# Kernel tuning notes

Hardware: AMD Instinct MI355X
Metric: run time of the kernel (lower is better)

Reference implementation:

```python
import jax, jax.numpy as jnp
import numpy as np

B, T, D = 1, 2048, 4096
H, HKV, HD = 32, 8, 128   # attention heads, KV heads, head_dim
R, RANK = 64, 16          # virtual KV tokens, LoRA rank
EPS = 1e-6


def setup_inputs() -> dict:
    key = jax.random.key(0)
    ks = jax.random.split(key, 12)
    inp = {
        "hidden_states": jax.random.normal(ks[0], (B, T, D), jnp.float32),
        "virtual_keys": jax.random.normal(ks[1], (B, HKV, R, HD), jnp.float32),
        "virtual_values": jax.random.normal(ks[2], (B, HKV, R, HD), jnp.float32),
        "Wq": jax.random.normal(ks[3], (D, H * HD), jnp.float32) * 0.02,
        "Wk": jax.random.normal(ks[4], (D, HKV * HD), jnp.float32) * 0.02,
        "Wv": jax.random.normal(ks[5], (D, HKV * HD), jnp.float32) * 0.02,
        "Wo": jax.random.normal(ks[6], (H * HD, D), jnp.float32) * 0.02,
        "q_norm_w": jnp.ones((HD,), jnp.float32),
        "k_norm_w": jnp.ones((HD,), jnp.float32),
        "lora_k_A": jax.random.normal(ks[7], (HD, RANK), jnp.float32) / np.sqrt(HD),
        "lora_k_B": jax.random.normal(ks[8], (RANK, HD), jnp.float32) * 0.02,
        "lora_v_A": jax.random.normal(ks[9], (HD, RANK), jnp.float32) / np.sqrt(HD),
        "lora_v_B": jax.random.normal(ks[10], (RANK, HD), jnp.float32) * 0.02,
        "scale_k": jnp.float32(0.1),
        "scale_v": jnp.float32(0.1),
    }
    # additive causal mask (B,1,T,T)
    neg = jnp.finfo(jnp.float32).min
    idx = jnp.arange(T)
    mask = jnp.where(idx[None, :] <= idx[:, None], 0.0, neg).astype(jnp.float32)
    inp["attention_mask"] = jnp.broadcast_to(mask[None, None], (B, 1, T, T))
    # rotary embeddings (T, HD)
    inv_freq = 1.0 / (10000.0 ** (jnp.arange(0, HD, 2, dtype=jnp.float32) / HD))
    freqs = jnp.outer(jnp.arange(T, dtype=jnp.float32), inv_freq)
    emb = jnp.concatenate([freqs, freqs], axis=-1)
    inp["cos"], inp["sin"] = jnp.cos(emb), jnp.sin(emb)
    return inp


def _rms_norm(x, w):
    xf = x.astype(jnp.float32)
    y = xf * jax.lax.rsqrt(jnp.mean(xf * xf, axis=-1, keepdims=True) + EPS)
    return y.astype(x.dtype) * w


def _rotate_half(x):
    x1, x2 = jnp.split(x, 2, axis=-1)
    return jnp.concatenate([-x2, x1], axis=-1)


def reference(hidden_states, virtual_keys, virtual_values, Wq, Wk, Wv, Wo,
              q_norm_w, k_norm_w, lora_k_A, lora_k_B, lora_v_A, lora_v_B,
              scale_k, scale_v, attention_mask, cos, sin):
    b, t, d = hidden_states.shape
    head_dim = q_norm_w.shape[0]
    scaling = head_dim ** -0.5

    # ---- KVLoRAAdapter: K' = K + s_k * (K @ A_k @ B_k), same for V ----
    vk = virtual_keys + scale_k * ((virtual_keys @ lora_k_A) @ lora_k_B)
    vv = virtual_values + scale_v * ((virtual_values @ lora_v_A) @ lora_v_B)

    # ---- Qwen3 attention projections with per-head RMSNorm ----
    q = _rms_norm((hidden_states @ Wq).reshape(b, t, -1, head_dim), q_norm_w).transpose(0, 2, 1, 3)  # (B,H,T,hd)
    k = _rms_norm((hidden_states @ Wk).reshape(b, t, -1, head_dim), k_norm_w).transpose(0, 2, 1, 3)  # (B,HKV,T,hd)
    v = (hidden_states @ Wv).reshape(b, t, -1, head_dim).transpose(0, 2, 1, 3)                       # (B,HKV,T,hd)

    # ---- RoPE ----
    c, s = cos[None, None], sin[None, None]
    q = q * c + _rotate_half(q) * s
    k = k * c + _rotate_half(k) * s

    # ---- prepend adapted virtual KV ----
    r = vk.shape[2]
    k = jnp.concatenate([vk.astype(k.dtype), k], axis=2)  # (B,HKV,r+T,hd)
    v = jnp.concatenate([vv.astype(v.dtype), v], axis=2)
    virtual_mask = jnp.zeros((b, 1, t, r), attention_mask.dtype)
    full_mask = jnp.concatenate([virtual_mask, attention_mask], axis=-1)  # (B,1,T,r+T)

    # ---- repeat_kv (GQA) ----
    groups = q.shape[1] // k.shape[1]
    k = jnp.repeat(k, groups, axis=1)
    v = jnp.repeat(v, groups, axis=1)

    # ---- attention ----
    attn = jnp.einsum('bhqd,bhkd->bhqk', q, k) * scaling + full_mask
    attn = jax.nn.softmax(attn.astype(jnp.float32), axis=-1).astype(q.dtype)
    out = jnp.einsum('bhqk,bhkd->bhqd', attn, v)
    out = out.transpose(0, 2, 1, 3).reshape(b, t, -1)
    return out @ Wo
```

## Files before the change

kernel.cpp:

```cpp
#include <hip/hip_runtime.h>

typedef unsigned short u16;
typedef __attribute__((ext_vector_type(8))) unsigned short u16x8;
typedef __attribute__((ext_vector_type(8))) short s16x8;
typedef __attribute__((ext_vector_type(4))) float f32x4;

__device__ __forceinline__ float bf2f(u16 v) {
    return __uint_as_float(((unsigned int)v) << 16);
}
__device__ __forceinline__ u16 f2bf(float f) {
    unsigned int u = __float_as_uint(f);
    return (u16)((u + 0x7FFFu + ((u >> 16) & 1u)) >> 16);
}

__global__ __launch_bounds__(256) void cvt_bf16_kernel(const float* __restrict__ src,
                                                       u16* __restrict__ dst, int n8) {
    int i = blockIdx.x * 256 + threadIdx.x;
    if (i >= n8) return;
    const float4* s4 = (const float4*)src;
    float4 a = s4[i * 2];
    float4 b = s4[i * 2 + 1];
    u16x8 o;
    o[0] = f2bf(a.x); o[1] = f2bf(a.y); o[2] = f2bf(a.z); o[3] = f2bf(a.w);
    o[4] = f2bf(b.x); o[5] = f2bf(b.y); o[6] = f2bf(b.z); o[7] = f2bf(b.w);
    *(u16x8*)(dst + (size_t)i * 8) = o;
}

__global__ __launch_bounds__(256) void tcvt_kernel(const float* __restrict__ src,
                                                   u16* __restrict__ dst, int K, int N) {
    __shared__ float T[32][33];
    int k0 = blockIdx.x * 32, n0 = blockIdx.y * 32;
    int r = threadIdx.x >> 5, c = threadIdx.x & 31;
#pragma unroll
    for (int it = 0; it < 4; ++it)
        T[it * 8 + r][c] = src[(size_t)(k0 + it * 8 + r) * N + n0 + c];
    __syncthreads();
#pragma unroll
    for (int it = 0; it < 4; ++it)
        dst[(size_t)(n0 + it * 8 + r) * K + k0 + c] = f2bf(T[c][it * 8 + r]);
}

__global__ __launch_bounds__(128) void lora_kv_kernel(
    const float* __restrict__ vk, const float* __restrict__ vv,
    const float* __restrict__ kA, const float* __restrict__ kB,
    const float* __restrict__ vA, const float* __restrict__ vB,
    const float* __restrict__ skp, const float* __restrict__ svp,
    u16* __restrict__ k_full, u16* __restrict__ v_t) {
    __shared__ float row[128];
    __shared__ float tv[16];
    int h = blockIdx.x >> 6, r = blockIdx.x & 63;
    int d = threadIdx.x;

    row[d] = vk[(size_t)(h * 64 + r) * 128 + d];
    __syncthreads();
    if (d < 16) {
        float acc = 0.f;
        for (int i = 0; i < 128; ++i) acc += row[i] * kA[i * 16 + d];
        tv[d] = acc;
    }
    __syncthreads();
    float acc = 0.f;
#pragma unroll
    for (int j = 0; j < 16; ++j) acc += tv[j] * kB[j * 128 + d];
    float outk = row[d] + skp[0] * acc;
    k_full[((size_t)h * 2112 + r) * 128 + d] = f2bf(outk);
    __syncthreads();

    row[d] = vv[(size_t)(h * 64 + r) * 128 + d];
    __syncthreads();
    if (d < 16) {
        float a2 = 0.f;
        for (int i = 0; i < 128; ++i) a2 += row[i] * vA[i * 16 + d];
        tv[d] = a2;
    }
    __syncthreads();
    float a3 = 0.f;
#pragma unroll
    for (int j = 0; j < 16; ++j) a3 += tv[j] * vB[j * 128 + d];
    float outv = row[d] + svp[0] * a3;
    v_t[((size_t)h * 128 + d) * 2112 + r] = f2bf(outv);
}

template <int OF32>
__global__ __launch_bounds__(256) void gemm_bt_kernel(const u16* __restrict__ A,
                                                      const u16* __restrict__ B,
                                                      void* __restrict__ Cv,
                                                      int M, int N, int K, int ldc) {
    __shared__ u16 As[128][40];
    __shared__ u16 Bs[128][40];
    int tid = threadIdx.x;
    int w = tid >> 6, l = tid & 63, lr = l & 15, lg = l >> 4;
    int m0 = blockIdx.x * 128, n0 = blockIdx.y * 128;
    int wr = (w >> 1) * 64, wc = (w & 1) * 64;
    int trow = tid >> 2, tcol = (tid & 3) * 8;

    const u16* Ag = A + (size_t)(m0 + trow) * K + tcol;
    const u16* Bg = B + (size_t)(n0 + trow) * K + tcol;

    u16x8 ra0 = *(const u16x8*)Ag;
    u16x8 ra1 = *(const u16x8*)(Ag + (size_t)64 * K);
    u16x8 rb0 = *(const u16x8*)Bg;
    u16x8 rb1 = *(const u16x8*)(Bg + (size_t)64 * K);

    f32x4 acc[4][4] = {};
    int NT = K >> 5;
    for (int kt = 0; kt < NT; ++kt) {
        __syncthreads();
        *(u16x8*)&As[trow][tcol] = ra0;
        *(u16x8*)&As[trow + 64][tcol] = ra1;
        *(u16x8*)&Bs[trow][tcol] = rb0;
        *(u16x8*)&Bs[trow + 64][tcol] = rb1;
        if (kt + 1 < NT) {
            int kb = (kt + 1) * 32;
            ra0 = *(const u16x8*)(Ag + kb);
            ra1 = *(const u16x8*)(Ag + kb + (size_t)64 * K);
            rb0 = *(const u16x8*)(Bg + kb);
            rb1 = *(const u16x8*)(Bg + kb + (size_t)64 * K);
        }
        __syncthreads();
        s16x8 af[4], bfr[4];
#pragma unroll
        for (int m = 0; m < 4; ++m) af[m] = *(const s16x8*)&As[wr + m * 16 + lr][lg * 8];
#pragma unroll
        for (int n = 0; n < 4; ++n) bfr[n] = *(const s16x8*)&Bs[wc + n * 16 + lr][lg * 8];
#pragma unroll
        for (int m = 0; m < 4; ++m)
#pragma unroll
            for (int n = 0; n < 4; ++n)
                acc[m][n] = __builtin_amdgcn_mfma_f32_16x16x32_bf16(af[m], bfr[n], acc[m][n], 0, 0, 0);
    }

#pragma unroll
    for (int m = 0; m < 4; ++m)
#pragma unroll
        for (int n = 0; n < 4; ++n)
#pragma unroll
            for (int j = 0; j < 4; ++j) {
                int row = m0 + wr + m * 16 + lg * 4 + j;
                int col = n0 + wc + n * 16 + lr;
                float v = acc[m][n][j];
                if (OF32)
                    ((float*)Cv)[(size_t)row * ldc + col] = v;
                else
                    ((u16*)Cv)[(size_t)row * ldc + col] = f2bf(v);
            }
}

__global__ __launch_bounds__(256) void qnorm_rope_kernel(const u16* __restrict__ qkv,
                                                         const float* __restrict__ qw,
                                                         const float* __restrict__ cosb,
                                                         const float* __restrict__ sinb,
                                                         u16* __restrict__ qf) {
    int w = threadIdx.x >> 6, l = threadIdx.x & 63;
    int idx = blockIdx.x * 4 + w;
    int t = idx >> 5, h = idx & 31;
    const u16* src = qkv + (size_t)t * 6144 + h * 128;
    float x1 = bf2f(src[l]), x2 = bf2f(src[l + 64]);
    float ss = x1 * x1 + x2 * x2;
#pragma unroll
    for (int d = 1; d < 64; d <<= 1) ss += __shfl_xor(ss, d, 64);
    float rinv = rsqrtf(ss * (1.0f / 128.0f) + 1e-6f);
    float y1 = x1 * rinv * qw[l], y2 = x2 * rinv * qw[l + 64];
    float c1 = cosb[t * 128 + l], s1 = sinb[t * 128 + l];
    float c2 = cosb[t * 128 + l + 64], s2 = sinb[t * 128 + l + 64];
    const float sc = 0.08838834764831845f;
    u16* dst = qf + (size_t)t * 4096 + h * 128;
    dst[l] = f2bf((y1 * c1 - y2 * s1) * sc);
    dst[l + 64] = f2bf((y2 * c2 + y1 * s2) * sc);
}

__global__ __launch_bounds__(256) void kvnorm_rope_kernel(const u16* __restrict__ qkv,
                                                          const float* __restrict__ kw,
                                                          const float* __restrict__ cosb,
                                                          const float* __restrict__ sinb,
                                                          u16* __restrict__ k_full,
                                                          u16* __restrict__ v_t) {
    __shared__ u16 VT[32][136];
    int h = blockIdx.x >> 6;
    int t0 = (blockIdx.x & 63) * 32;
    int tid = threadIdx.x;
    int w = tid >> 6, l = tid & 63;

    for (int it = 0; it < 8; ++it) {
        int t = t0 + w * 8 + it;
        const u16* src = qkv + (size_t)t * 6144 + 4096 + h * 128;
        float x1 = bf2f(src[l]), x2 = bf2f(src[l + 64]);
        float ss = x1 * x1 + x2 * x2;
#pragma unroll
        for (int d = 1; d < 64; d <<= 1) ss += __shfl_xor(ss, d, 64);
        float rinv = rsqrtf(ss * (1.0f / 128.0f) + 1e-6f);
        float y1 = x1 * rinv * kw[l], y2 = x2 * rinv * kw[l + 64];
        float c1 = cosb[t * 128 + l], s1 = sinb[t * 128 + l];
        float c2 = cosb[t * 128 + l + 64], s2 = sinb[t * 128 + l + 64];
        u16* dst = k_full + ((size_t)h * 2112 + 64 + t) * 128;
        dst[l] = f2bf(y1 * c1 - y2 * s1);
        dst[l + 64] = f2bf(y2 * c2 + y1 * s2);
    }

    {
        int tr = tid >> 3, c0 = (tid & 7) * 16;
        const u16* src = qkv + (size_t)(t0 + tr) * 6144 + 5120 + h * 128 + c0;
        *(u16x8*)&VT[tr][c0] = *(const u16x8*)src;
        *(u16x8*)&VT[tr][c0 + 8] = *(const u16x8*)(src + 8);
    }
    __syncthreads();
    {
        int d = tid >> 1, th = (tid & 1) * 16;
        u16x8 a, b;
#pragma unroll
        for (int i = 0; i < 8; ++i) { a[i] = VT[th + i][d]; b[i] = VT[th + 8 + i][d]; }
        u16* dst = v_t + ((size_t)h * 128 + d) * 2112 + 64 + t0 + th;
        *(u16x8*)dst = a;
        *(u16x8*)(dst + 8) = b;
    }
}

__global__ __launch_bounds__(256) void attn_kernel(const u16* __restrict__ qf,
                                                   const u16* __restrict__ k_full,
                                                   const u16* __restrict__ v_t,
                                                   u16* __restrict__ attn_out) {
    __shared__ u16 Ks[64][136];
    __shared__ u16 Vs[128][72];
    __shared__ u16 Pw[4][16][72];

    int h = blockIdx.x >> 5;
    int qt = 31 - (blockIdx.x & 31);
    int q0 = qt * 64;
    int kvh = h >> 2;
    int tid = threadIdx.x, w = tid >> 6, l = tid & 63;
    int lr = l & 15, lg = l >> 4;

    s16x8 qfr[4];
    const u16* qbase = qf + (size_t)(q0 + w * 16 + lr) * 4096 + h * 128 + lg * 8;
#pragma unroll
    for (int ks = 0; ks < 4; ++ks) qfr[ks] = *(const s16x8*)(qbase + ks * 32);

    f32x4 o[8] = {};
    float mrun[4], lrun[4];
#pragma unroll
    for (int j = 0; j < 4; ++j) { mrun[j] = -1e30f; lrun[j] = 0.f; }

    int nt = q0 / 64 + 2;
    const u16* Kg = k_full + (size_t)kvh * 2112 * 128;
    const u16* Vg = v_t + (size_t)kvh * 128 * 2112;

    for (int tile = 0; tile < nt; ++tile) {
        int kv0 = tile * 64;
        __syncthreads();
#pragma unroll
        for (int c = 0; c < 4; ++c) {
            int kk = tid + c * 256;
            int row = kk >> 4, col = (kk & 15) * 8;
            *(u16x8*)&Ks[row][col] = *(const u16x8*)(Kg + (size_t)(kv0 + row) * 128 + col);
        }
#pragma unroll
        for (int c = 0; c < 4; ++c) {
            int kk = tid + c * 256;
            int row = kk >> 3, col = (kk & 7) * 8;
            *(u16x8*)&Vs[row][col] = *(const u16x8*)(Vg + (size_t)row * 2112 + kv0 + col);
        }
        __syncthreads();

        f32x4 s[4] = {};
#pragma unroll
        for (int ks = 0; ks < 4; ++ks) {
#pragma unroll
            for (int n = 0; n < 4; ++n) {
                s16x8 b = *(const s16x8*)&Ks[n * 16 + lr][ks * 32 + lg * 8];
                s[n] = __builtin_amdgcn_mfma_f32_16x16x32_bf16(qfr[ks], b, s[n], 0, 0, 0);
            }
        }

        if (tile == nt - 1) {
#pragma unroll
            for (int n = 0; n < 4; ++n) {
                int kvi = kv0 + n * 16 + lr;
                if (kvi >= 64) {
                    int kreal = kvi - 64;
#pragma unroll
                    for (int j = 0; j < 4; ++j) {
                        int qi = q0 + w * 16 + lg * 4 + j;
                        if (kreal > qi) s[n][j] = -1e30f;
                    }
                }
            }
        }

#pragma unroll
        for (int j = 0; j < 4; ++j) {
            float mx = fmaxf(fmaxf(s[0][j], s[1][j]), fmaxf(s[2][j], s[3][j]));
            mx = fmaxf(mx, __shfl_xor(mx, 1, 64));
            mx = fmaxf(mx, __shfl_xor(mx, 2, 64));
            mx = fmaxf(mx, __shfl_xor(mx, 4, 64));
            mx = fmaxf(mx, __shfl_xor(mx, 8, 64));
            float mnew = fmaxf(mrun[j], mx);
            float scl = __expf(mrun[j] - mnew);
            mrun[j] = mnew;
            lrun[j] *= scl;
#pragma unroll
            for (int nf = 0; nf < 8; ++nf) o[nf][j] *= scl;
            float psum = 0.f;
#pragma unroll
            for (int n = 0; n < 4; ++n) {
                float p = __expf(s[n][j] - mnew);
                s[n][j] = p;
                psum += p;
            }
            lrun[j] += psum;
        }

#pragma unroll
        for (int n = 0; n < 4; ++n)
#pragma unroll
            for (int j = 0; j < 4; ++j)
                Pw[w][lg * 4 + j][n * 16 + lr] = f2bf(s[n][j]);

#pragma unroll
        for (int ks2 = 0; ks2 < 2; ++ks2) {
            s16x8 pa = *(const s16x8*)&Pw[w][lr][ks2 * 32 + lg * 8];
#pragma unroll
            for (int nf = 0; nf < 8; ++nf) {
                s16x8 vb = *(const s16x8*)&Vs[nf * 16 + lr][ks2 * 32 + lg * 8];
                o[nf] = __builtin_amdgcn_mfma_f32_16x16x32_bf16(pa, vb, o[nf], 0, 0, 0);
            }
        }
    }

    float rinv[4];
#pragma unroll
    for (int j = 0; j < 4; ++j) {
        float ls = lrun[j];
        ls += __shfl_xor(ls, 1, 64);
        ls += __shfl_xor(ls, 2, 64);
        ls += __shfl_xor(ls, 4, 64);
        ls += __shfl_xor(ls, 8, 64);
        rinv[j] = 1.0f / ls;
    }
#pragma unroll
    for (int nf = 0; nf < 8; ++nf)
#pragma unroll
        for (int j = 0; j < 4; ++j) {
            int row = q0 + w * 16 + lg * 4 + j;
            int col = h * 128 + nf * 16 + lr;
            attn_out[(size_t)row * 4096 + col] = f2bf(o[nf][j] * rinv[j]);
        }
}

extern "C" void kernel_launch(void* const* d_in, const int* in_sizes, int n_in,
                              void* d_out, int out_size, void* d_ws, size_t ws_size,
                              hipStream_t stream) {
    const float* hidden = (const float*)d_in[0];
    const float* vkeys = (const float*)d_in[1];
    const float* vvals = (const float*)d_in[2];
    const float* Wq = (const float*)d_in[3];
    const float* Wk = (const float*)d_in[4];
    const float* Wv = (const float*)d_in[5];
    const float* Wo = (const float*)d_in[6];
    const float* qnw = (const float*)d_in[7];
    const float* knw = (const float*)d_in[8];
    const float* lkA = (const float*)d_in[9];
    const float* lkB = (const float*)d_in[10];
    const float* lvA = (const float*)d_in[11];
    const float* lvB = (const float*)d_in[12];
    const float* skp = (const float*)d_in[13];
    const float* svp = (const float*)d_in[14];
    const float* cosb = (const float*)d_in[16];
    const float* sinb = (const float*)d_in[17];

    char* ws = (char*)d_ws;
    u16* hid_bf = (u16*)(ws);
    u16* WqT    = (u16*)(ws + 16777216);
    u16* WkT    = (u16*)(ws + 50331648);
    u16* WvT    = (u16*)(ws + 58720256);
    u16* WoT    = (u16*)(ws + 67108864);
    u16* qkv    = (u16*)(ws + 100663296);
    u16* qfin   = (u16*)(ws + 125829120);
    u16* kfull  = (u16*)(ws + 142606336);
    u16* vt     = (u16*)(ws + 146931712);
    u16* attn_o = hid_bf;

    cvt_bf16_kernel<<<4096, 256, 0, stream>>>(hidden, hid_bf, 1048576);
    tcvt_kernel<<<dim3(128, 128), 256, 0, stream>>>(Wq, WqT, 4096, 4096);
    tcvt_kernel<<<dim3(128, 32), 256, 0, stream>>>(Wk, WkT, 4096, 1024);
    tcvt_kernel<<<dim3(128, 32), 256, 0, stream>>>(Wv, WvT, 4096, 1024);
    tcvt_kernel<<<dim3(128, 128), 256, 0, stream>>>(Wo, WoT, 4096, 4096);

    lora_kv_kernel<<<512, 128, 0, stream>>>(vkeys, vvals, lkA, lkB, lvA, lvB, skp, svp,
                                            kfull, vt);

    gemm_bt_kernel<0><<<dim3(16, 48), 256, 0, stream>>>(hid_bf, WqT, qkv, 2048, 6144, 4096, 6144);

    qnorm_rope_kernel<<<16384, 256, 0, stream>>>(qkv, qnw, cosb, sinb, qfin);
    kvnorm_rope_kernel<<<512, 256, 0, stream>>>(qkv, knw, cosb, sinb, kfull, vt);

    attn_kernel<<<1024, 256, 0, stream>>>(qfin, kfull, vt, attn_o);

    gemm_bt_kernel<1><<<dim3(16, 32), 256, 0, stream>>>(attn_o, WoT, d_out, 2048, 4096, 4096, 4096);
}
```

Baseline: 657.6 us.

## Use direct-to-LDS double-buffered GEMM loads and rebalance flash attention

The GEMM now copies global memory straight into a double-buffered LDS tile with global_load_lds, replacing the register-staged single buffer, so the next tile loads while the current one computes. The attention kernel pairs a long and a short causal query tile per block to even out work, and swaps padded LDS rows for XOR-swizzled layouts to avoid bank conflicts. It also folds log2(e) into the Q scale so it can use exp2f, and skips the running-max rescale when the max has grown by no more than a set threshold. This risks LDS bank conflicts in the unpadded GEMM tiles, leaves half as many attention blocks, and relies on the lazy-rescale threshold staying numerically safe.

```diff
diff --git a/kernel.cpp b/kernel.cpp
--- a/kernel.cpp
+++ b/kernel.cpp
@@ -5,12 +5,18 @@
 typedef __attribute__((ext_vector_type(8))) short s16x8;
 typedef __attribute__((ext_vector_type(4))) float f32x4;
 
+typedef __attribute__((address_space(1))) void gvoid;
+typedef __attribute__((address_space(3))) void lvoid;
+
 __device__ __forceinline__ float bf2f(u16 v) {
     return __uint_as_float(((unsigned int)v) << 16);
 }
 __device__ __forceinline__ u16 f2bf(float f) {
     unsigned int u = __float_as_uint(f);
     return (u16)((u + 0x7FFFu + ((u >> 16) & 1u)) >> 16);
+}
+__device__ __forceinline__ void gload16(const void* g, void* l) {
+    __builtin_amdgcn_global_load_lds((gvoid*)g, (lvoid*)l, 16, 0, 0);
 }
 
 __global__ __launch_bounds__(256) void cvt_bf16_kernel(const float* __restrict__ src,
@@ -86,49 +92,55 @@
                                                       const u16* __restrict__ B,
                                                       void* __restrict__ Cv,
                                                       int M, int N, int K, int ldc) {
-    __shared__ u16 As[128][40];
-    __shared__ u16 Bs[128][40];
+    __shared__ u16 As[2][128][32];
+    __shared__ u16 Bs[2][128][32];
     int tid = threadIdx.x;
     int w = tid >> 6, l = tid & 63, lr = l & 15, lg = l >> 4;
     int m0 = blockIdx.x * 128, n0 = blockIdx.y * 128;
     int wr = (w >> 1) * 64, wc = (w & 1) * 64;
-    int trow = tid >> 2, tcol = (tid & 3) * 8;
-
-    const u16* Ag = A + (size_t)(m0 + trow) * K + tcol;
-    const u16* Bg = B + (size_t)(n0 + trow) * K + tcol;
-
-    u16x8 ra0 = *(const u16x8*)Ag;
-    u16x8 ra1 = *(const u16x8*)(Ag + (size_t)64 * K);
-    u16x8 rb0 = *(const u16x8*)Bg;
-    u16x8 rb1 = *(const u16x8*)(Bg + (size_t)64 * K);
+    int srow = tid >> 2, scol = (tid & 3) * 8;
+
+    const u16* Ag = A + (size_t)(m0 + srow) * K + scol;
+    const u16* Bg = B + (size_t)(n0 + srow) * K + scol;
+    size_t rstep = (size_t)64 * K;
 
     f32x4 acc[4][4] = {};
     int NT = K >> 5;
-    for (int kt = 0; kt < NT; ++kt) {
+
+#define STAGE_G(buf, kt)                                       \
+    do {                                                       \
+        int koff = (kt) * 32;                                  \
+        gload16(Ag + koff, &As[buf][srow][scol]);              \
+        gload16(Ag + koff + rstep, &As[buf][srow + 64][scol]); \
+        gload16(Bg + koff, &Bs[buf][srow][scol]);              \
+        gload16(Bg + koff + rstep, &Bs[buf][srow + 64][scol]); \
+    } while (0)
+
+#define COMPUTE_G(buf)                                                                     \
+    do {                                                                                   \
+        s16x8 af[4], bfr[4];                                                               \
+        _Pragma("unroll") for (int m = 0; m < 4; ++m)                                      \
+            af[m] = *(const s16x8*)&As[buf][wr + m * 16 + lr][lg * 8];                     \
+        _Pragma("unroll") for (int n = 0; n < 4; ++n)                                      \
+            bfr[n] = *(const s16x8*)&Bs[buf][wc + n * 16 + lr][lg * 8];                    \
+        _Pragma("unroll") for (int m = 0; m < 4; ++m)                                      \
+            _Pragma("unroll") for (int n = 0; n < 4; ++n)                                  \
+                acc[m][n] = __builtin_amdgcn_mfma_f32_16x16x32_bf16(af[m], bfr[n],         \
+                                                                    acc[m][n], 0, 0, 0);  \
+    } while (0)
+
+    STAGE_G(0, 0);
+    __syncthreads();
+    for (int kt = 0; kt < NT; kt += 2) {
+        if (kt + 1 < NT) STAGE_G(1, kt + 1);
+        COMPUTE_G(0);
         __syncthreads();
-        *(u16x8*)&As[trow][tcol] = ra0;
-        *(u16x8*)&As[trow + 64][tcol] = ra1;
-        *(u16x8*)&Bs[trow][tcol] = rb0;
-        *(u16x8*)&Bs[trow + 64][tcol] = rb1;
-        if (kt + 1 < NT) {
-            int kb = (kt + 1) * 32;
-            ra0 = *(const u16x8*)(Ag + kb);
-            ra1 = *(const u16x8*)(Ag + kb + (size_t)64 * K);
-            rb0 = *(const u16x8*)(Bg + kb);
-            rb1 = *(const u16x8*)(Bg + kb + (size_t)64 * K);
-        }
+        if (kt + 2 < NT) STAGE_G(0, kt + 2);
+        COMPUTE_G(1);
         __syncthreads();
-        s16x8 af[4], bfr[4];
-#pragma unroll
-        for (int m = 0; m < 4; ++m) af[m] = *(const s16x8*)&As[wr + m * 16 + lr][lg * 8];
-#pragma unroll
-        for (int n = 0; n < 4; ++n) bfr[n] = *(const s16x8*)&Bs[wc + n * 16 + lr][lg * 8];
-#pragma unroll
-        for (int m = 0; m < 4; ++m)
-#pragma unroll
-            for (int n = 0; n < 4; ++n)
-                acc[m][n] = __builtin_amdgcn_mfma_f32_16x16x32_bf16(af[m], bfr[n], acc[m][n], 0, 0, 0);
-    }
+    }
+#undef STAGE_G
+#undef COMPUTE_G
 
 #pragma unroll
     for (int m = 0; m < 4; ++m)
@@ -163,7 +175,7 @@
     float y1 = x1 * rinv * qw[l], y2 = x2 * rinv * qw[l + 64];
     float c1 = cosb[t * 128 + l], s1 = sinb[t * 128 + l];
     float c2 = cosb[t * 128 + l + 64], s2 = sinb[t * 128 + l + 64];
-    const float sc = 0.08838834764831845f;
+    const float sc = 0.08838834764831845f * 1.4426950408889634f;
     u16* dst = qf + (size_t)t * 4096 + h * 128;
     dst[l] = f2bf((y1 * c1 - y2 * s1) * sc);
     dst[l + 64] = f2bf((y2 * c2 + y1 * s2) * sc);
@@ -219,131 +231,152 @@
                                                    const u16* __restrict__ k_full,
                                                    const u16* __restrict__ v_t,
                                                    u16* __restrict__ attn_out) {
-    __shared__ u16 Ks[64][136];
-    __shared__ u16 Vs[128][72];
-    __shared__ u16 Pw[4][16][72];
-
-    int h = blockIdx.x >> 5;
-    int qt = 31 - (blockIdx.x & 31);
-    int q0 = qt * 64;
+    __shared__ u16 Ks[64][128];
+    __shared__ u16 Vs[128][64];
+    __shared__ u16 Pw[4][16][64];
+
+    int h = blockIdx.x >> 4;
+    int pr = blockIdx.x & 15;
     int kvh = h >> 2;
     int tid = threadIdx.x, w = tid >> 6, l = tid & 63;
     int lr = l & 15, lg = l >> 4;
-
-    s16x8 qfr[4];
-    const u16* qbase = qf + (size_t)(q0 + w * 16 + lr) * 4096 + h * 128 + lg * 8;
-#pragma unroll
-    for (int ks = 0; ks < 4; ++ks) qfr[ks] = *(const s16x8*)(qbase + ks * 32);
-
-    f32x4 o[8] = {};
-    float mrun[4], lrun[4];
-#pragma unroll
-    for (int j = 0; j < 4; ++j) { mrun[j] = -1e30f; lrun[j] = 0.f; }
-
-    int nt = q0 / 64 + 2;
     const u16* Kg = k_full + (size_t)kvh * 2112 * 128;
     const u16* Vg = v_t + (size_t)kvh * 128 * 2112;
 
-    for (int tile = 0; tile < nt; ++tile) {
-        int kv0 = tile * 64;
-        __syncthreads();
-#pragma unroll
-        for (int c = 0; c < 4; ++c) {
-            int kk = tid + c * 256;
-            int row = kk >> 4, col = (kk & 15) * 8;
-            *(u16x8*)&Ks[row][col] = *(const u16x8*)(Kg + (size_t)(kv0 + row) * 128 + col);
+    for (int seg = 0; seg < 2; ++seg) {
+        int qt = seg ? pr : 31 - pr;
+        int q0 = qt * 64;
+
+        s16x8 qfr[4];
+        const u16* qbase = qf + (size_t)(q0 + w * 16 + lr) * 4096 + h * 128 + lg * 8;
+#pragma unroll
+        for (int ks = 0; ks < 4; ++ks) qfr[ks] = *(const s16x8*)(qbase + ks * 32);
+
+        f32x4 o[8] = {};
+        float mrun[4], lrun[4];
+#pragma unroll
+        for (int j = 0; j < 4; ++j) { mrun[j] = -1e30f; lrun[j] = 0.f; }
+
+        int nt = qt + 2;
+        for (int tile = 0; tile < nt; ++tile) {
+            int kv0 = tile * 64;
+            __syncthreads();
+#pragma unroll
+            for (int c = 0; c < 4; ++c) {
+                int kk = tid + c * 256;
+                int row = kk >> 4, col = (kk & 15) * 8;
+                *(u16x8*)&Ks[row][col ^ ((row & 7) << 3)] =
+                    *(const u16x8*)(Kg + (size_t)(kv0 + row) * 128 + col);
+            }
+#pragma unroll
+            for (int c = 0; c < 4; ++c) {
+                int kk = tid + c * 256;
+                int row = kk >> 3, col = (kk & 7) * 8;
+                *(u16x8*)&Vs[row][col ^ ((row & 7) << 3)] =
+                    *(const u16x8*)(Vg + (size_t)row * 2112 + kv0 + col);
+            }
+            __syncthreads();
+
+            f32x4 s[4] = {};
+#pragma unroll
+            for (int ks = 0; ks < 4; ++ks) {
+#pragma unroll
+                for (int n = 0; n < 4; ++n) {
+                    s16x8 b = *(const s16x8*)&Ks[n * 16 + lr][(ks * 32 + lg * 8) ^ ((lr & 7) << 3)];
+                    s[n] = __builtin_amdgcn_mfma_f32_16x16x32_bf16(qfr[ks], b, s[n], 0, 0, 0);
+                }
+            }
+
+            if (tile == nt - 1) {
+#pragma unroll
+                for (int n = 0; n < 4; ++n) {
+                    int kvi = kv0 + n * 16 + lr;
+                    if (kvi >= 64) {
+                        int kreal = kvi - 64;
+#pragma unroll
+                        for (int j = 0; j < 4; ++j) {
+                            int qi = q0 + w * 16 + lg * 4 + j;
+                            if (kreal > qi) s[n][j] = -1e30f;
+                        }
+                    }
+                }
+            }
+
+            float tmx[4];
+            float growth = -3.0e38f;
+#pragma unroll
+            for (int j = 0; j < 4; ++j) {
+                float mx = fmaxf(fmaxf(s[0][j], s[1][j]), fmaxf(s[2][j], s[3][j]));
+                mx = fmaxf(mx, __shfl_xor(mx, 1, 64));
+                mx = fmaxf(mx, __shfl_xor(mx, 2, 64));
+                mx = fmaxf(mx, __shfl_xor(mx, 4, 64));
+                mx = fmaxf(mx, __shfl_xor(mx, 8, 64));
+                tmx[j] = mx;
+                growth = fmaxf(growth, mx - mrun[j]);
+            }
+            if (!__all(growth <= 11.5f)) {
+#pragma unroll
+                for (int j = 0; j < 4; ++j) {
+                    float mnew = fmaxf(mrun[j], tmx[j]);
+                    float scl = exp2f(mrun[j] - mnew);
+                    mrun[j] = mnew;
+                    lrun[j] *= scl;
+#pragma unroll
+                    for (int nf = 0; nf < 8; ++nf) o[nf][j] *= scl;
+                }
+            }
+#pragma unroll
+            for (int j = 0; j < 4; ++j) {
+                float psum = 0.f;
+#pragma unroll
+                for (int n = 0; n < 4; ++n) {
+                    float p = exp2f(s[n][j] - mrun[j]);
+                    s[n][j] = p;
+                    psum += p;
+                }
+                lrun[j] += psum;
+            }
+
+#pragma unroll
+            for (int n = 0; n < 4; ++n)
+#pragma unroll
+                for (int j = 0; j < 4; ++j) {
+                    int prow = lg * 4 + j;
+                    int pcol = n * 16 + lr;
+                    int pswz = (pcol & 7) | ((((pcol >> 3) ^ prow) & 7) << 3);
+                    Pw[w][prow][pswz] = f2bf(s[n][j]);
+                }
+
+#pragma unroll
+            for (int ks2 = 0; ks2 < 2; ++ks2) {
+                s16x8 pa = *(const s16x8*)&Pw[w][lr][(ks2 * 32 + lg * 8) ^ ((lr & 7) << 3)];
+#pragma unroll
+                for (int nf = 0; nf < 8; ++nf) {
+                    s16x8 vb = *(const s16x8*)&Vs[nf * 16 + lr][(ks2 * 32 + lg * 8) ^ ((lr & 7) << 3)];
+                    o[nf] = __builtin_amdgcn_mfma_f32_16x16x32_bf16(pa, vb, o[nf], 0, 0, 0);
+                }
+            }
         }
-#pragma unroll
-        for (int c = 0; c < 4; ++c) {
-            int kk = tid + c * 256;
-            int row = kk >> 3, col = (kk & 7) * 8;
-            *(u16x8*)&Vs[row][col] = *(const u16x8*)(Vg + (size_t)row * 2112 + kv0 + col);
+
+        float rinv[4];
+#pragma unroll
+        for (int j = 0; j < 4; ++j) {
+            float ls = lrun[j];
+            ls += __shfl_xor(ls, 1, 64);
+            ls += __shfl_xor(ls, 2, 64);
+            ls += __shfl_xor(ls, 4, 64);
+            ls += __shfl_xor(ls, 8, 64);
+            rinv[j] = 1.0f / ls;
         }
-        __syncthreads();
-
-        f32x4 s[4] = {};
-#pragma unroll
-        for (int ks = 0; ks < 4; ++ks) {
-#pragma unroll
-            for (int n = 0; n < 4; ++n) {
-                s16x8 b = *(const s16x8*)&Ks[n * 16 + lr][ks * 32 + lg * 8];
-                s[n] = __builtin_amdgcn_mfma_f32_16x16x32_bf16(qfr[ks], b, s[n], 0, 0, 0);
-            }
-        }
-
-        if (tile == nt - 1) {
-#pragma unroll
-            for (int n = 0; n < 4; ++n) {
-                int kvi = kv0 + n * 16 + lr;
-                if (kvi >= 64) {
-                    int kreal = kvi - 64;
-#pragma unroll
-                    for (int j = 0; j < 4; ++j) {
-                        int qi = q0 + w * 16 + lg * 4 + j;
-                        if (kreal > qi) s[n][j] = -1e30f;
-                    }
-                }
-            }
-        }
-
-#pragma unroll
-        for (int j = 0; j < 4; ++j) {
-            float mx = fmaxf(fmaxf(s[0][j], s[1][j]), fmaxf(s[2][j], s[3][j]));
-            mx = fmaxf(mx, __shfl_xor(mx, 1, 64));
-            mx = fmaxf(mx, __shfl_xor(mx, 2, 64));
-            mx = fmaxf(mx, __shfl_xor(mx, 4, 64));
-            mx = fmaxf(mx, __shfl_xor(mx, 8, 64));
-            float mnew = fmaxf(mrun[j], mx);
-            float scl = __expf(mrun[j] - mnew);
-            mrun[j] = mnew;
-            lrun[j] *= scl;
-#pragma unroll
-            for (int nf = 0; nf < 8; ++nf) o[nf][j] *= scl;
-            float psum = 0.f;
-#pragma unroll
-            for (int n = 0; n < 4; ++n) {
-                float p = __expf(s[n][j] - mnew);
-                s[n][j] = p;
-                psum += p;
-            }
-            lrun[j] += psum;
-        }
-
-#pragma unroll
-        for (int n = 0; n < 4; ++n)
-#pragma unroll
-            for (int j = 0; j < 4; ++j)
-                Pw[w][lg * 4 + j][n * 16 + lr] = f2bf(s[n][j]);
-
-#pragma unroll
-        for (int ks2 = 0; ks2 < 2; ++ks2) {
-            s16x8 pa = *(const s16x8*)&Pw[w][lr][ks2 * 32 + lg * 8];
-#pragma unroll
-            for (int nf = 0; nf < 8; ++nf) {
-                s16x8 vb = *(const s16x8*)&Vs[nf * 16 + lr][ks2 * 32 + lg * 8];
-                o[nf] = __builtin_amdgcn_mfma_f32_16x16x32_bf16(pa, vb, o[nf], 0, 0, 0);
-            }
-        }
-    }
-
-    float rinv[4];
-#pragma unroll
-    for (int j = 0; j < 4; ++j) {
-        float ls = lrun[j];
-        ls += __shfl_xor(ls, 1, 64);
-        ls += __shfl_xor(ls, 2, 64);
-        ls += __shfl_xor(ls, 4, 64);
-        ls += __shfl_xor(ls, 8, 64);
-        rinv[j] = 1.0f / ls;
-    }
-#pragma unroll
-    for (int nf = 0; nf < 8; ++nf)
-#pragma unroll
-        for (int j = 0; j < 4; ++j) {
-            int row = q0 + w * 16 + lg * 4 + j;
-            int col = h * 128 + nf * 16 + lr;
-            attn_out[(size_t)row * 4096 + col] = f2bf(o[nf][j] * rinv[j]);
-        }
+#pragma unroll
+        for (int nf = 0; nf < 8; ++nf)
+#pragma unroll
+            for (int j = 0; j < 4; ++j) {
+                int row = q0 + w * 16 + lg * 4 + j;
+                int col = h * 128 + nf * 16 + lr;
+                attn_out[(size_t)row * 4096 + col] = f2bf(o[nf][j] * rinv[j]);
+            }
+    }
 }
 
 extern "C" void kernel_launch(void* const* d_in, const int* in_sizes, int n_in,
@@ -393,7 +426,7 @@
     qnorm_rope_kernel<<<16384, 256, 0, stream>>>(qkv, qnw, cosb, sinb, qfin);
     kvnorm_rope_kernel<<<512, 256, 0, stream>>>(qkv, knw, cosb, sinb, kfull, vt);
 
-    attn_kernel<<<1024, 256, 0, stream>>>(qfin, kfull, vt, attn_o);
+    attn_kernel<<<512, 256, 0, stream>>>(qfin, kfull, vt, attn_o);
 
     gemm_bt_kernel<1><<<dim3(16, 32), 256, 0, stream>>>(attn_o, WoT, d_out, 2048, 4096, 4096, 4096);
 }
```

New measurement: 589.4 us. 10.4% less time.
